# Kernel optimization log

Measured on AMD Instinct MI355X. Metric: run time of the kernel, lower is better.

Reference implementation:

```python
import jax, jax.numpy as jnp
import numpy as np

ALPHA = 0.01  # leakyrelu negative slope


def setup_inputs() -> dict:
    key = jax.random.key(0)
    k1, k2, k3 = jax.random.split(key, 3)
    B, N, F_in, F_out = 32, 1024, 256, 256
    inp = jax.random.normal(k1, (B, N, F_in), dtype=jnp.float32)
    # xavier_uniform-like scale, gain=1.414
    lim_W = 1.414 * np.sqrt(6.0 / (F_in + F_out))
    W = jax.random.uniform(k2, (F_in, F_out), dtype=jnp.float32, minval=-lim_W, maxval=lim_W)
    lim_a = 1.414 * np.sqrt(6.0 / (2 * F_out + 1))
    a = jax.random.uniform(k3, (2 * F_out, 1), dtype=jnp.float32, minval=-lim_a, maxval=lim_a)
    return {"inp": inp, "W": W, "a": a}


def reference(inp, W, a):
    # h: [B, N, F_out]
    h = jnp.matmul(inp, W)
    F_out = W.shape[1]
    # Additive attention: score[b,i,j] = leakyrelu(h[b,i]@a1 + h[b,j]@a2).
    # Mathematically identical to cat([h_i, h_j]) @ a without materializing
    # the O(N^2 * 2F) a_input tensor.
    a1 = a[:F_out, 0]  # [F_out]
    a2 = a[F_out:, 0]  # [F_out]
    f1 = jnp.einsum('bnf,f->bn', h, a1)  # [B, N]
    f2 = jnp.einsum('bnf,f->bn', h, a2)  # [B, N]
    e = f1[:, :, None] + f2[:, None, :]  # [B, N, N]
    e = jnp.where(e > 0, e, ALPHA * e)   # leakyrelu
    attention = jax.nn.softmax(e, axis=-1)
    # dropout omitted (deterministic eval-mode reference)
    h_prime = jnp.matmul(attention, h)   # [B, N, F_out]
    return jax.nn.elu(h_prime)
```

## Files before the change

### kernel.cpp

```cpp
#include <hip/hip_runtime.h>
#include <hip/hip_bf16.h>

typedef unsigned short u16;
typedef unsigned int u32;
typedef __attribute__((ext_vector_type(4))) float f32x4;
typedef __attribute__((ext_vector_type(8))) short s16x8;
typedef __attribute__((ext_vector_type(4))) unsigned short u16x4;
typedef __attribute__((ext_vector_type(8))) unsigned short u16x8;

#define LRELU(x) ((x) > 0.f ? (x) : 0.01f * (x))

static __device__ __forceinline__ u16 f2bf(float x) {
    u32 u = __float_as_uint(x);
    return (u16)((u + 0x7fffu + ((u >> 16) & 1u)) >> 16);
}
static __device__ __forceinline__ float bf2f(u16 h) { return __uint_as_float((u32)h << 16); }

__global__ void k_prep(const float* __restrict__ W, const float* __restrict__ a,
                       u16* __restrict__ Wt_hi, u16* __restrict__ Wt_lo,
                       float* __restrict__ w1, float* __restrict__ w2) {
    int i = blockIdx.x, t = threadIdx.x;
    float x = W[i * 256 + t];
    float p1 = x * a[t];
    float p2 = x * a[256 + t];
#pragma unroll
    for (int off = 1; off < 64; off <<= 1) {
        p1 += __shfl_xor(p1, off);
        p2 += __shfl_xor(p2, off);
    }
    __shared__ float s1[4], s2[4];
    if ((t & 63) == 0) { s1[t >> 6] = p1; s2[t >> 6] = p2; }
    __syncthreads();
    if (t == 0) {
        w1[i] = s1[0] + s1[1] + s1[2] + s1[3];
        w2[i] = s2[0] + s2[1] + s2[2] + s2[3];
    }
    float y = W[t * 256 + i];
    u16 hi = f2bf(y);
    Wt_hi[i * 256 + t] = hi;
    Wt_lo[i * 256 + t] = f2bf(y - bf2f(hi));
}

__global__ void k_f(const float* __restrict__ inp, const float* __restrict__ w1,
                    const float* __restrict__ w2, float* __restrict__ f1,
                    float* __restrict__ f2) {
    __shared__ float sw1[256], sw2[256];
    int t = threadIdx.x;
    sw1[t] = w1[t];
    sw2[t] = w2[t];
    __syncthreads();
    int wv = t >> 6, l = t & 63;
    f32x4 c1 = *(const f32x4*)&sw1[l * 4];
    f32x4 c2 = *(const f32x4*)&sw2[l * 4];
    for (int it = 0; it < 16; ++it) {
        int row = blockIdx.x * 64 + wv * 16 + it;
        f32x4 v = *(const f32x4*)&inp[row * 256 + l * 4];
        float d1 = v.x * c1.x + v.y * c1.y + v.z * c1.z + v.w * c1.w;
        float d2 = v.x * c2.x + v.y * c2.y + v.z * c2.z + v.w * c2.w;
#pragma unroll
        for (int off = 1; off < 64; off <<= 1) {
            d1 += __shfl_xor(d1, off);
            d2 += __shfl_xor(d2, off);
        }
        if (l == 0) { f1[row] = d1; f2[row] = d2; }
    }
}

__global__ void k_m(const float* __restrict__ f2, float* __restrict__ Mb) {
    int b = blockIdx.x, t = threadIdx.x;
    float m = -1e30f;
#pragma unroll
    for (int j = 0; j < 4; ++j) m = fmaxf(m, f2[b * 1024 + t + j * 256]);
#pragma unroll
    for (int off = 1; off < 64; off <<= 1) m = fmaxf(m, __shfl_xor(m, off));
    __shared__ float s[4];
    if ((t & 63) == 0) s[t >> 6] = m;
    __syncthreads();
    if (t == 0) Mb[b] = fmaxf(fmaxf(s[0], s[1]), fmaxf(s[2], s[3]));
}

__global__ __launch_bounds__(256, 2) void k_h(const float* __restrict__ inp,
                                              const u16* __restrict__ Wt_hi,
                                              const u16* __restrict__ Wt_lo,
                                              u16* __restrict__ ht_hi,
                                              u16* __restrict__ ht_lo) {
    int t = threadIdx.x, w = t >> 6, l = t & 63, lr = l & 15, lk = l >> 4;
    int n0 = blockIdx.x * 64;
    int bb = n0 >> 10, nb0 = n0 & 1023;

    f32x4 acc[4][4];
#pragma unroll
    for (int i = 0; i < 4; ++i)
#pragma unroll
        for (int j = 0; j < 4; ++j)
#pragma unroll
            for (int r = 0; r < 4; ++r) acc[i][j][r] = 0.f;

    for (int kt = 0; kt < 8; ++kt) {
        int k0 = kt * 32 + lk * 8;
        s16x8 ah[4], al[4];
#pragma unroll
        for (int it = 0; it < 4; ++it) {
            int f = w * 64 + it * 16 + lr;
            ah[it] = *(const s16x8*)&Wt_hi[f * 256 + k0];
            al[it] = *(const s16x8*)&Wt_lo[f * 256 + k0];
        }
        s16x8 bh[4], bl[4];
#pragma unroll
        for (int ci = 0; ci < 4; ++ci) {
            int n = n0 + ci * 16 + lr;
            f32x4 v0 = *(const f32x4*)&inp[n * 256 + k0];
            f32x4 v1 = *(const f32x4*)&inp[n * 256 + k0 + 4];
            u16x8 hv, lv;
#pragma unroll
            for (int j = 0; j < 4; ++j) {
                u16 h0 = f2bf(v0[j]);
                hv[j] = h0;
                lv[j] = f2bf(v0[j] - bf2f(h0));
                u16 h1 = f2bf(v1[j]);
                hv[j + 4] = h1;
                lv[j + 4] = f2bf(v1[j] - bf2f(h1));
            }
            bh[ci] = *(s16x8*)&hv;
            bl[ci] = *(s16x8*)&lv;
        }
#pragma unroll
        for (int it = 0; it < 4; ++it)
#pragma unroll
            for (int ci = 0; ci < 4; ++ci) {
                acc[it][ci] = __builtin_amdgcn_mfma_f32_16x16x32_bf16(ah[it], bh[ci], acc[it][ci], 0, 0, 0);
                acc[it][ci] = __builtin_amdgcn_mfma_f32_16x16x32_bf16(ah[it], bl[ci], acc[it][ci], 0, 0, 0);
                acc[it][ci] = __builtin_amdgcn_mfma_f32_16x16x32_bf16(al[it], bh[ci], acc[it][ci], 0, 0, 0);
            }
    }
#pragma unroll
    for (int it = 0; it < 4; ++it)
#pragma unroll
        for (int ci = 0; ci < 4; ++ci) {
            int col = nb0 + ci * 16 + lr;
#pragma unroll
            for (int r = 0; r < 4; ++r) {
                int F = w * 64 + it * 16 + lk * 4 + r;
                float x = acc[it][ci][r];
                u16 hh = f2bf(x);
                size_t o = (size_t)(bb * 256 + F) * 1024 + col;
                ht_hi[o] = hh;
                ht_lo[o] = f2bf(x - bf2f(hh));
            }
        }
}

__global__ __launch_bounds__(512, 4) void k_attn(const u16* __restrict__ ht_hi,
                                                 const u16* __restrict__ ht_lo,
                                                 const float* __restrict__ f1,
                                                 const float* __restrict__ f2,
                                                 const float* __restrict__ Mb,
                                                 float* __restrict__ out) {
    __shared__ float sf2[1024];
    __shared__ u16 P[2][4][4][512];
    __shared__ float rs[128];
    int t = threadIdx.x, w = t >> 6, l = t & 63, lr = l & 15, lk = l >> 4;
    int wf = w & 3, wr = w >> 2;
    int g = blockIdx.x;
    int xcd = g & 7, idx = g >> 3;
    int b = xcd * 4 + (idx >> 4);
    int i0 = (idx & 15) * 64;

    if (t < 256) *(f32x4*)&sf2[t * 4] = *(const f32x4*)&f2[b * 1024 + t * 4];
    float Mv = Mb[b];
    int rgp = wf;
    int sh = wr;
    float f1v = f1[b * 1024 + i0 + rgp * 16 + lr];
    float miv = LRELU(f1v + Mv);
    float lsum = 0.f;
    const u16* Hh = ht_hi + (size_t)b * 262144;
    const u16* Hl = ht_lo + (size_t)b * 262144;

    auto computeP = [&](int cc2, int buf2) {
#pragma unroll
        for (int ss = 0; ss < 2; ++ss) {
            int s = sh * 2 + ss;
            int jb = cc2 * 128 + s * 32 + lk * 8;
            f32x4 fa = *(const f32x4*)&sf2[jb];
            f32x4 fb = *(const f32x4*)&sf2[jb + 4];
            u16x8 pv;
#pragma unroll
            for (int jj = 0; jj < 8; ++jj) {
                float fv = (jj < 4) ? fa[jj] : fb[jj - 4];
                float e = LRELU(f1v + fv);
                float p = __expf(e - miv);
                lsum += p;
                pv[jj] = f2bf(p);
            }
            *(u16x8*)&P[buf2][rgp][s][l * 8] = pv;
        }
    };

    f32x4 acc[2][4];
#pragma unroll
    for (int i = 0; i < 2; ++i)
#pragma unroll
        for (int j = 0; j < 4; ++j)
#pragma unroll
            for (int r = 0; r < 4; ++r) acc[i][j][r] = 0.f;

    __syncthreads();
    computeP(0, 0);

    for (int cc = 0; cc < 8; ++cc) {
        __syncthreads();
        if (cc < 7) computeP(cc + 1, (cc + 1) & 1);
        int buf = cc & 1;
#pragma unroll
        for (int s = 0; s < 4; ++s) {
            int jcol = cc * 128 + s * 32 + lk * 8;
            s16x8 pf[2];
            pf[0] = *(const s16x8*)&P[buf][wr * 2][s][l * 8];
            pf[1] = *(const s16x8*)&P[buf][wr * 2 + 1][s][l * 8];
#pragma unroll
            for (int ci = 0; ci < 4; ++ci) {
                int f = wf * 64 + ci * 16 + lr;
                s16x8 bh = *(const s16x8*)&Hh[(size_t)f * 1024 + jcol];
                s16x8 bl = *(const s16x8*)&Hl[(size_t)f * 1024 + jcol];
                __builtin_amdgcn_s_setprio(1);
                acc[0][ci] = __builtin_amdgcn_mfma_f32_16x16x32_bf16(pf[0], bh, acc[0][ci], 0, 0, 0);
                acc[0][ci] = __builtin_amdgcn_mfma_f32_16x16x32_bf16(pf[0], bl, acc[0][ci], 0, 0, 0);
                acc[1][ci] = __builtin_amdgcn_mfma_f32_16x16x32_bf16(pf[1], bh, acc[1][ci], 0, 0, 0);
                acc[1][ci] = __builtin_amdgcn_mfma_f32_16x16x32_bf16(pf[1], bl, acc[1][ci], 0, 0, 0);
                __builtin_amdgcn_s_setprio(0);
            }
        }
    }

    lsum += __shfl_xor(lsum, 16);
    lsum += __shfl_xor(lsum, 32);
    if (l < 16) rs[w * 16 + lr] = lsum;
    __syncthreads();

#pragma unroll
    for (int it = 0; it < 2; ++it) {
        int rg = wr * 2 + it;
        f32x4 s1 = *(const f32x4*)&rs[rg * 16 + lk * 4];
        f32x4 s2 = *(const f32x4*)&rs[(rg + 4) * 16 + lk * 4];
        f32x4 sums = s1 + s2;
#pragma unroll
        for (int ci = 0; ci < 4; ++ci) {
            int col = wf * 64 + ci * 16 + lr;
            int rowg = b * 1024 + i0 + rg * 16 + lk * 4;
#pragma unroll
            for (int r = 0; r < 4; ++r) {
                float v = acc[it][ci][r] / sums[r];
                v = v > 0.f ? v : (__expf(v) - 1.f);
                out[(size_t)(rowg + r) * 256 + col] = v;
            }
        }
    }
}

extern "C" void kernel_launch(void* const* d_in, const int* in_sizes, int n_in,
                              void* d_out, int out_size, void* d_ws, size_t ws_size,
                              hipStream_t stream) {
    const float* inp = (const float*)d_in[0];
    const float* W = (const float*)d_in[1];
    const float* a = (const float*)d_in[2];
    float* out = (float*)d_out;

    char* ws = (char*)d_ws;
    u16* ht_hi = (u16*)(ws + 0);
    u16* ht_lo = (u16*)(ws + 16777216);
    u16* Wt_hi = (u16*)(ws + 33554432);
    u16* Wt_lo = (u16*)(ws + 33685504);
    float* w1 = (float*)(ws + 33816576);
    float* w2 = (float*)(ws + 33817600);
    float* f1 = (float*)(ws + 33818624);
    float* f2 = (float*)(ws + 33949696);
    float* Mb = (float*)(ws + 34080768);

    k_prep<<<256, 256, 0, stream>>>(W, a, Wt_hi, Wt_lo, w1, w2);
    k_f<<<512, 256, 0, stream>>>(inp, w1, w2, f1, f2);
    k_m<<<32, 256, 0, stream>>>(f2, Mb);
    k_h<<<512, 256, 0, stream>>>(inp, Wt_hi, Wt_lo, ht_hi, ht_lo);
    k_attn<<<512, 512, 0, stream>>>(ht_hi, ht_lo, f1, f2, Mb, out);
}
```

Before: 250.4 us.

## Switch to fp16 MFMA, single-precision h, fuse f1/f2 into h kernel

Replaces the bf16 hi/lo split with fp16. The h matmul keeps a three-term hi/lo split, but h is now stored as a single fp16 tensor, so the attention matmul uses one MFMA per product instead of two and reads half the H bytes. The f1/f2 projection kernel is folded into the h GEMM, which removes a separate pass over the input. Both kernels are retiled to smaller blocks with twice as many blocks. The risks are the loss of precision in h and possible fp16 overflow or underflow of the softmax probabilities.

```diff
diff --git a/kernel.cpp b/kernel.cpp
--- a/kernel.cpp
+++ b/kernel.cpp
@@ -4,17 +4,22 @@
 typedef unsigned short u16;
 typedef unsigned int u32;
 typedef __attribute__((ext_vector_type(4))) float f32x4;
-typedef __attribute__((ext_vector_type(8))) short s16x8;
-typedef __attribute__((ext_vector_type(4))) unsigned short u16x4;
+typedef __attribute__((ext_vector_type(8))) _Float16 f16x8;
 typedef __attribute__((ext_vector_type(8))) unsigned short u16x8;
 
 #define LRELU(x) ((x) > 0.f ? (x) : 0.01f * (x))
 
-static __device__ __forceinline__ u16 f2bf(float x) {
-    u32 u = __float_as_uint(x);
-    return (u16)((u + 0x7fffu + ((u >> 16) & 1u)) >> 16);
-}
-static __device__ __forceinline__ float bf2f(u16 h) { return __uint_as_float((u32)h << 16); }
+static __device__ __forceinline__ u16 f2h(float x) {
+    _Float16 h = (_Float16)x;
+    u16 r;
+    __builtin_memcpy(&r, &h, 2);
+    return r;
+}
+static __device__ __forceinline__ float h2f(u16 v) {
+    _Float16 h;
+    __builtin_memcpy(&h, &v, 2);
+    return (float)h;
+}
 
 __global__ void k_prep(const float* __restrict__ W, const float* __restrict__ a,
                        u16* __restrict__ Wt_hi, u16* __restrict__ Wt_lo,
@@ -36,34 +41,9 @@
         w2[i] = s2[0] + s2[1] + s2[2] + s2[3];
     }
     float y = W[t * 256 + i];
-    u16 hi = f2bf(y);
+    u16 hi = f2h(y);
     Wt_hi[i * 256 + t] = hi;
-    Wt_lo[i * 256 + t] = f2bf(y - bf2f(hi));
-}
-
-__global__ void k_f(const float* __restrict__ inp, const float* __restrict__ w1,
-                    const float* __restrict__ w2, float* __restrict__ f1,
-                    float* __restrict__ f2) {
-    __shared__ float sw1[256], sw2[256];
-    int t = threadIdx.x;
-    sw1[t] = w1[t];
-    sw2[t] = w2[t];
-    __syncthreads();
-    int wv = t >> 6, l = t & 63;
-    f32x4 c1 = *(const f32x4*)&sw1[l * 4];
-    f32x4 c2 = *(const f32x4*)&sw2[l * 4];
-    for (int it = 0; it < 16; ++it) {
-        int row = blockIdx.x * 64 + wv * 16 + it;
-        f32x4 v = *(const f32x4*)&inp[row * 256 + l * 4];
-        float d1 = v.x * c1.x + v.y * c1.y + v.z * c1.z + v.w * c1.w;
-        float d2 = v.x * c2.x + v.y * c2.y + v.z * c2.z + v.w * c2.w;
-#pragma unroll
-        for (int off = 1; off < 64; off <<= 1) {
-            d1 += __shfl_xor(d1, off);
-            d2 += __shfl_xor(d2, off);
-        }
-        if (l == 0) { f1[row] = d1; f2[row] = d2; }
-    }
+    Wt_lo[i * 256 + t] = f2h(y - h2f(hi));
 }
 
 __global__ void k_m(const float* __restrict__ f2, float* __restrict__ Mb) {
@@ -79,107 +59,126 @@
     if (t == 0) Mb[b] = fmaxf(fmaxf(s[0], s[1]), fmaxf(s[2], s[3]));
 }
 
-__global__ __launch_bounds__(256, 2) void k_h(const float* __restrict__ inp,
+__global__ __launch_bounds__(256, 4) void k_h(const float* __restrict__ inp,
                                               const u16* __restrict__ Wt_hi,
                                               const u16* __restrict__ Wt_lo,
-                                              u16* __restrict__ ht_hi,
-                                              u16* __restrict__ ht_lo) {
+                                              const float* __restrict__ w1,
+                                              const float* __restrict__ w2,
+                                              u16* __restrict__ ht,
+                                              float* __restrict__ f1,
+                                              float* __restrict__ f2) {
+    __shared__ float sw1[256], sw2[256];
     int t = threadIdx.x, w = t >> 6, l = t & 63, lr = l & 15, lk = l >> 4;
-    int n0 = blockIdx.x * 64;
+    sw1[t] = w1[t];
+    sw2[t] = w2[t];
+    __syncthreads();
+    int n0 = blockIdx.x * 32;
     int bb = n0 >> 10, nb0 = n0 & 1023;
 
-    f32x4 acc[4][4];
+    f32x4 acc[4][2];
 #pragma unroll
     for (int i = 0; i < 4; ++i)
 #pragma unroll
-        for (int j = 0; j < 4; ++j)
+        for (int j = 0; j < 2; ++j)
 #pragma unroll
             for (int r = 0; r < 4; ++r) acc[i][j][r] = 0.f;
+    float d1[2] = {0.f, 0.f}, d2[2] = {0.f, 0.f};
 
     for (int kt = 0; kt < 8; ++kt) {
         int k0 = kt * 32 + lk * 8;
-        s16x8 ah[4], al[4];
+        f16x8 ah[4], al[4];
 #pragma unroll
         for (int it = 0; it < 4; ++it) {
             int f = w * 64 + it * 16 + lr;
-            ah[it] = *(const s16x8*)&Wt_hi[f * 256 + k0];
-            al[it] = *(const s16x8*)&Wt_lo[f * 256 + k0];
-        }
-        s16x8 bh[4], bl[4];
-#pragma unroll
-        for (int ci = 0; ci < 4; ++ci) {
+            ah[it] = *(const f16x8*)&Wt_hi[f * 256 + k0];
+            al[it] = *(const f16x8*)&Wt_lo[f * 256 + k0];
+        }
+        f32x4 c1a = *(const f32x4*)&sw1[k0];
+        f32x4 c1b = *(const f32x4*)&sw1[k0 + 4];
+        f32x4 c2a = *(const f32x4*)&sw2[k0];
+        f32x4 c2b = *(const f32x4*)&sw2[k0 + 4];
+#pragma unroll
+        for (int ci = 0; ci < 2; ++ci) {
             int n = n0 + ci * 16 + lr;
             f32x4 v0 = *(const f32x4*)&inp[n * 256 + k0];
             f32x4 v1 = *(const f32x4*)&inp[n * 256 + k0 + 4];
+            d1[ci] += v0.x * c1a.x + v0.y * c1a.y + v0.z * c1a.z + v0.w * c1a.w +
+                      v1.x * c1b.x + v1.y * c1b.y + v1.z * c1b.z + v1.w * c1b.w;
+            d2[ci] += v0.x * c2a.x + v0.y * c2a.y + v0.z * c2a.z + v0.w * c2a.w +
+                      v1.x * c2b.x + v1.y * c2b.y + v1.z * c2b.z + v1.w * c2b.w;
             u16x8 hv, lv;
 #pragma unroll
             for (int j = 0; j < 4; ++j) {
-                u16 h0 = f2bf(v0[j]);
+                u16 h0 = f2h(v0[j]);
                 hv[j] = h0;
-                lv[j] = f2bf(v0[j] - bf2f(h0));
-                u16 h1 = f2bf(v1[j]);
+                lv[j] = f2h(v0[j] - h2f(h0));
+                u16 h1 = f2h(v1[j]);
                 hv[j + 4] = h1;
-                lv[j + 4] = f2bf(v1[j] - bf2f(h1));
-            }
-            bh[ci] = *(s16x8*)&hv;
-            bl[ci] = *(s16x8*)&lv;
-        }
-#pragma unroll
-        for (int it = 0; it < 4; ++it)
-#pragma unroll
-            for (int ci = 0; ci < 4; ++ci) {
-                acc[it][ci] = __builtin_amdgcn_mfma_f32_16x16x32_bf16(ah[it], bh[ci], acc[it][ci], 0, 0, 0);
-                acc[it][ci] = __builtin_amdgcn_mfma_f32_16x16x32_bf16(ah[it], bl[ci], acc[it][ci], 0, 0, 0);
-                acc[it][ci] = __builtin_amdgcn_mfma_f32_16x16x32_bf16(al[it], bh[ci], acc[it][ci], 0, 0, 0);
-            }
+                lv[j + 4] = f2h(v1[j] - h2f(h1));
+            }
+            f16x8 bh = *(f16x8*)&hv, bl = *(f16x8*)&lv;
+#pragma unroll
+            for (int it = 0; it < 4; ++it) {
+                acc[it][ci] = __builtin_amdgcn_mfma_f32_16x16x32_f16(ah[it], bh, acc[it][ci], 0, 0, 0);
+                acc[it][ci] = __builtin_amdgcn_mfma_f32_16x16x32_f16(ah[it], bl, acc[it][ci], 0, 0, 0);
+                acc[it][ci] = __builtin_amdgcn_mfma_f32_16x16x32_f16(al[it], bh, acc[it][ci], 0, 0, 0);
+            }
+        }
+    }
+#pragma unroll
+    for (int ci = 0; ci < 2; ++ci) {
+        d1[ci] += __shfl_xor(d1[ci], 16);
+        d1[ci] += __shfl_xor(d1[ci], 32);
+        d2[ci] += __shfl_xor(d2[ci], 16);
+        d2[ci] += __shfl_xor(d2[ci], 32);
+    }
+    if (w == 0 && l < 16) {
+#pragma unroll
+        for (int ci = 0; ci < 2; ++ci) {
+            f1[n0 + ci * 16 + l] = d1[ci];
+            f2[n0 + ci * 16 + l] = d2[ci];
+        }
     }
 #pragma unroll
     for (int it = 0; it < 4; ++it)
 #pragma unroll
-        for (int ci = 0; ci < 4; ++ci) {
+        for (int ci = 0; ci < 2; ++ci) {
             int col = nb0 + ci * 16 + lr;
 #pragma unroll
             for (int r = 0; r < 4; ++r) {
                 int F = w * 64 + it * 16 + lk * 4 + r;
-                float x = acc[it][ci][r];
-                u16 hh = f2bf(x);
-                size_t o = (size_t)(bb * 256 + F) * 1024 + col;
-                ht_hi[o] = hh;
-                ht_lo[o] = f2bf(x - bf2f(hh));
-            }
-        }
-}
-
-__global__ __launch_bounds__(512, 4) void k_attn(const u16* __restrict__ ht_hi,
-                                                 const u16* __restrict__ ht_lo,
+                ht[(size_t)(bb * 256 + F) * 1024 + col] = f2h(acc[it][ci][r]);
+            }
+        }
+}
+
+__global__ __launch_bounds__(256, 4) void k_attn(const u16* __restrict__ ht,
                                                  const float* __restrict__ f1,
                                                  const float* __restrict__ f2,
                                                  const float* __restrict__ Mb,
                                                  float* __restrict__ out) {
     __shared__ float sf2[1024];
-    __shared__ u16 P[2][4][4][512];
-    __shared__ float rs[128];
+    __shared__ u16 P[2][2][4][512];
+    __shared__ float rs[64];
     int t = threadIdx.x, w = t >> 6, l = t & 63, lr = l & 15, lk = l >> 4;
-    int wf = w & 3, wr = w >> 2;
     int g = blockIdx.x;
     int xcd = g & 7, idx = g >> 3;
-    int b = xcd * 4 + (idx >> 4);
-    int i0 = (idx & 15) * 64;
-
-    if (t < 256) *(f32x4*)&sf2[t * 4] = *(const f32x4*)&f2[b * 1024 + t * 4];
+    int b = xcd * 4 + (idx >> 5);
+    int i0 = (idx & 31) * 32;
+
+    *(f32x4*)&sf2[t * 4] = *(const f32x4*)&f2[b * 1024 + t * 4];
     float Mv = Mb[b];
-    int rgp = wf;
-    int sh = wr;
+    int rgp = w & 1;
+    int jh = w >> 1;
     float f1v = f1[b * 1024 + i0 + rgp * 16 + lr];
     float miv = LRELU(f1v + Mv);
     float lsum = 0.f;
-    const u16* Hh = ht_hi + (size_t)b * 262144;
-    const u16* Hl = ht_lo + (size_t)b * 262144;
+    const u16* H = ht + (size_t)b * 262144;
 
     auto computeP = [&](int cc2, int buf2) {
 #pragma unroll
         for (int ss = 0; ss < 2; ++ss) {
-            int s = sh * 2 + ss;
+            int s = jh * 2 + ss;
             int jb = cc2 * 128 + s * 32 + lk * 8;
             f32x4 fa = *(const f32x4*)&sf2[jb];
             f32x4 fb = *(const f32x4*)&sf2[jb + 4];
@@ -190,7 +189,7 @@
                 float e = LRELU(f1v + fv);
                 float p = __expf(e - miv);
                 lsum += p;
-                pv[jj] = f2bf(p);
+                pv[jj] = f2h(p);
             }
             *(u16x8*)&P[buf2][rgp][s][l * 8] = pv;
         }
@@ -214,21 +213,17 @@
 #pragma unroll
         for (int s = 0; s < 4; ++s) {
             int jcol = cc * 128 + s * 32 + lk * 8;
-            s16x8 pf[2];
-            pf[0] = *(const s16x8*)&P[buf][wr * 2][s][l * 8];
-            pf[1] = *(const s16x8*)&P[buf][wr * 2 + 1][s][l * 8];
+            f16x8 pf0 = *(const f16x8*)&P[buf][0][s][l * 8];
+            f16x8 pf1 = *(const f16x8*)&P[buf][1][s][l * 8];
+            __builtin_amdgcn_s_setprio(1);
 #pragma unroll
             for (int ci = 0; ci < 4; ++ci) {
-                int f = wf * 64 + ci * 16 + lr;
-                s16x8 bh = *(const s16x8*)&Hh[(size_t)f * 1024 + jcol];
-                s16x8 bl = *(const s16x8*)&Hl[(size_t)f * 1024 + jcol];
-                __builtin_amdgcn_s_setprio(1);
-                acc[0][ci] = __builtin_amdgcn_mfma_f32_16x16x32_bf16(pf[0], bh, acc[0][ci], 0, 0, 0);
-                acc[0][ci] = __builtin_amdgcn_mfma_f32_16x16x32_bf16(pf[0], bl, acc[0][ci], 0, 0, 0);
-                acc[1][ci] = __builtin_amdgcn_mfma_f32_16x16x32_bf16(pf[1], bh, acc[1][ci], 0, 0, 0);
-                acc[1][ci] = __builtin_amdgcn_mfma_f32_16x16x32_bf16(pf[1], bl, acc[1][ci], 0, 0, 0);
-                __builtin_amdgcn_s_setprio(0);
-            }
+                int f = w * 64 + ci * 16 + lr;
+                f16x8 bh = *(const f16x8*)&H[(size_t)f * 1024 + jcol];
+                acc[0][ci] = __builtin_amdgcn_mfma_f32_16x16x32_f16(pf0, bh, acc[0][ci], 0, 0, 0);
+                acc[1][ci] = __builtin_amdgcn_mfma_f32_16x16x32_f16(pf1, bh, acc[1][ci], 0, 0, 0);
+            }
+            __builtin_amdgcn_s_setprio(0);
         }
     }
 
@@ -239,14 +234,13 @@
 
 #pragma unroll
     for (int it = 0; it < 2; ++it) {
-        int rg = wr * 2 + it;
-        f32x4 s1 = *(const f32x4*)&rs[rg * 16 + lk * 4];
-        f32x4 s2 = *(const f32x4*)&rs[(rg + 4) * 16 + lk * 4];
+        f32x4 s1 = *(const f32x4*)&rs[it * 16 + lk * 4];
+        f32x4 s2 = *(const f32x4*)&rs[(it + 2) * 16 + lk * 4];
         f32x4 sums = s1 + s2;
 #pragma unroll
         for (int ci = 0; ci < 4; ++ci) {
-            int col = wf * 64 + ci * 16 + lr;
-            int rowg = b * 1024 + i0 + rg * 16 + lk * 4;
+            int col = w * 64 + ci * 16 + lr;
+            int rowg = b * 1024 + i0 + it * 16 + lk * 4;
 #pragma unroll
             for (int r = 0; r < 4; ++r) {
                 float v = acc[it][ci][r] / sums[r];
@@ -266,19 +260,17 @@
     float* out = (float*)d_out;
 
     char* ws = (char*)d_ws;
-    u16* ht_hi = (u16*)(ws + 0);
-    u16* ht_lo = (u16*)(ws + 16777216);
-    u16* Wt_hi = (u16*)(ws + 33554432);
-    u16* Wt_lo = (u16*)(ws + 33685504);
-    float* w1 = (float*)(ws + 33816576);
-    float* w2 = (float*)(ws + 33817600);
-    float* f1 = (float*)(ws + 33818624);
-    float* f2 = (float*)(ws + 33949696);
-    float* Mb = (float*)(ws + 34080768);
+    u16* ht = (u16*)(ws + 0);
+    u16* Wt_hi = (u16*)(ws + 16777216);
+    u16* Wt_lo = (u16*)(ws + 16908288);
+    float* w1 = (float*)(ws + 17039360);
+    float* w2 = (float*)(ws + 17040384);
+    float* f1 = (float*)(ws + 17041408);
+    float* f2 = (float*)(ws + 17172480);
+    float* Mb = (float*)(ws + 17303552);
 
     k_prep<<<256, 256, 0, stream>>>(W, a, Wt_hi, Wt_lo, w1, w2);
-    k_f<<<512, 256, 0, stream>>>(inp, w1, w2, f1, f2);
+    k_h<<<1024, 256, 0, stream>>>(inp, Wt_hi, Wt_lo, w1, w2, ht, f1, f2);
     k_m<<<32, 256, 0, stream>>>(f2, Mb);
-    k_h<<<512, 256, 0, stream>>>(inp, Wt_hi, Wt_lo, ht_hi, ht_lo);
-    k_attn<<<512, 512, 0, stream>>>(ht_hi, ht_lo, f1, f2, Mb, out);
-}
+    k_attn<<<1024, 256, 0, stream>>>(ht, f1, f2, Mb, out);
+}
```

Result: faster. 201.2 us (-19.6%).
